# Optimization experiments

Measured on AMD Instinct MI355X. Metric: run time of the kernel, lower is better.

## Reference

```python
import jax, jax.numpy as jnp
import numpy as np

HIDDEN = 4096
NUM_HEADS = 32
HEAD_DIM = HIDDEN // NUM_HEADS  # 128, used only as softmax scale
CACHE_LEN = 100
BATCH = 8192


def setup_inputs() -> dict:
    key = jax.random.key(0)
    ks = jax.random.split(key, 7)
    return {
        "x": jax.random.normal(ks[0], (BATCH, HIDDEN), dtype=jnp.float32),
        "q_w": jax.random.normal(ks[1], (HIDDEN, HIDDEN), dtype=jnp.float32) * (1.0 / np.sqrt(HIDDEN)),
        "q_b": jax.random.normal(ks[2], (HIDDEN,), dtype=jnp.float32) * 0.01,
        "k_cache": jax.random.normal(ks[3], (CACHE_LEN, HIDDEN), dtype=jnp.float32),
        "v_cache": jax.random.normal(ks[4], (CACHE_LEN, HIDDEN), dtype=jnp.float32),
        "out_w": jax.random.normal(ks[5], (HIDDEN, HIDDEN), dtype=jnp.float32) * (1.0 / np.sqrt(HIDDEN)),
        "out_b": jax.random.normal(ks[6], (HIDDEN,), dtype=jnp.float32) * 0.01,
    }


def reference(x, q_w, q_b, k_cache, v_cache, out_w, out_b):
    # q_proj: torch Linear -> x @ W^T + b
    q = x @ q_w.T + q_b                                   # [N, H]
    # concat one zero row onto each cache (kv_len = CACHE_LEN + 1)
    k = jnp.concatenate([k_cache, jnp.zeros_like(k_cache[:1])], axis=0)  # [L+1, H]
    v = jnp.concatenate([v_cache, jnp.zeros_like(v_cache[:1])], axis=0)  # [L+1, H]
    scale = 1.0 / np.sqrt(HEAD_DIM).astype(np.float32)
    scores = (q @ k.T) * scale                            # [N, L+1]
    weights = jax.nn.softmax(scores, axis=-1)
    attn = weights @ v                                    # [N, H]
    return attn @ out_w.T + out_b                         # [N, H]
```

## Files before the change

### kernel.cpp

```cpp
#include <hip/hip_runtime.h>
#include <cstdio>

typedef __attribute__((ext_vector_type(8))) short short8;
typedef __attribute__((ext_vector_type(4))) float f32x4;


__device__ __forceinline__ unsigned short bf16r(float f) {
  union { float f; unsigned int u; } x; x.f = f;
  unsigned int r = x.u + 0x7fffu + ((x.u >> 16) & 1u);
  return (unsigned short)(r >> 16);
}

__device__ __forceinline__ float bf16f(unsigned short h) {
  union { unsigned int u; float f; } x; x.u = ((unsigned int)h) << 16;
  return x.f;
}

__device__ __forceinline__ void gload_lds16(const void* g, void* l) {
  __builtin_amdgcn_global_load_lds((const __attribute__((address_space(1))) void*)g,
                                   (__attribute__((address_space(3))) void*)l,
                                   16, 0, 0);
}

__device__ __forceinline__ short8 pack_bf16(float4 f0, float4 f1) {
  short8 h;
  h[0] = (short)bf16r(f0.x); h[1] = (short)bf16r(f0.y);
  h[2] = (short)bf16r(f0.z); h[3] = (short)bf16r(f0.w);
  h[4] = (short)bf16r(f1.x); h[5] = (short)bf16r(f1.y);
  h[6] = (short)bf16r(f1.z); h[7] = (short)bf16r(f1.w);
  return h;
}


__global__ void prep(const float* __restrict__ kc, const float* __restrict__ vc,
                     const float* __restrict__ qb,
                     unsigned short* __restrict__ kpad, unsigned short* __restrict__ vpad,
                     float* __restrict__ sbias) {
  const int b = blockIdx.x, tid = threadIdx.x;
  if (b < 4096) {
    const bool isK = b < 2048;
    const int bb = isK ? b : b - 2048;
    int idx = bb * 256 + tid;
    int row = idx >> 12;
    const float* src = isK ? kc : vc;
    float v = (row < 100) ? src[idx] : 0.f;
    (isK ? kpad : vpad)[idx] = bf16r(v);
  } else {
    const int wave = tid >> 6, lane = tid & 63;
    const int l = (b - 4096) * 4 + wave;
    float s = 0.f;
    if (l < 100) {
      for (int i = lane * 4; i < 4096; i += 256) {
        float4 k = *reinterpret_cast<const float4*>(kc + (size_t)l * 4096 + i);
        float4 q = *reinterpret_cast<const float4*>(qb + i);
        s += k.x * q.x + k.y * q.y + k.z * q.z + k.w * q.w;
      }
    }
    #pragma unroll
    for (int off = 1; off < 64; off <<= 1) s += __shfl_xor(s, off);
    if (lane == 0) sbias[l] = s;
  }
}


__device__ __forceinline__ void kq_fused_body(const unsigned short* __restrict__ Kp,
                                              const float* __restrict__ Qw,
                                              float* __restrict__ Cpart,
                                              int H, int jchunk, int js, int itile,
                                              char* smem) {
  unsigned short (*Ak)[32] = (unsigned short (*)[32])smem;
  float (*Ts)[129] = (float (*)[129])(smem + 8192);

  const int tid = threadIdx.x, wave = tid >> 6, lane = tid & 63;
  const int wm = wave >> 1, wn = wave & 1;
  const int j0 = js * jchunk;
  const int i0 = itile * 128;

  const int sr = wave * 16 + (lane >> 2);
  const int sc = (lane & 3) << 3;
  const unsigned short* Kp0 = Kp + (size_t)sr * H + j0 + sc;
  const unsigned short* Kp1 = Kp + (size_t)(64 + sr) * H + j0 + sc;
  unsigned short* AD0 = &Ak[wave * 16][0];
  unsigned short* AD1 = &Ak[64 + wave * 16][0];

  const int tj = tid >> 3;
  const int tc = (tid & 7) * 16;
  const float* Qp = Qw + (size_t)(j0 + tj) * H + i0 + tc;

  const int fr = lane & 15;
  const int kq = lane >> 4;

  f32x4 acc[4][4] = {};

  for (int jj = 0; jj < jchunk; jj += 32) {
    gload_lds16(Kp0 + jj, AD0);
    gload_lds16(Kp1 + jj, AD1);
    {
      const float* q = Qp + (size_t)jj * H;
      float4 v0 = *reinterpret_cast<const float4*>(q);
      float4 v1 = *reinterpret_cast<const float4*>(q + 4);
      float4 v2 = *reinterpret_cast<const float4*>(q + 8);
      float4 v3 = *reinterpret_cast<const float4*>(q + 12);
      Ts[tj][tc + 0]  = v0.x; Ts[tj][tc + 1]  = v0.y; Ts[tj][tc + 2]  = v0.z; Ts[tj][tc + 3]  = v0.w;
      Ts[tj][tc + 4]  = v1.x; Ts[tj][tc + 5]  = v1.y; Ts[tj][tc + 6]  = v1.z; Ts[tj][tc + 7]  = v1.w;
      Ts[tj][tc + 8]  = v2.x; Ts[tj][tc + 9]  = v2.y; Ts[tj][tc + 10] = v2.z; Ts[tj][tc + 11] = v2.w;
      Ts[tj][tc + 12] = v3.x; Ts[tj][tc + 13] = v3.y; Ts[tj][tc + 14] = v3.z; Ts[tj][tc + 15] = v3.w;
    }
    __syncthreads();

    short8 av[4];
    #pragma unroll
    for (int mi = 0; mi < 4; ++mi)
      av[mi] = *reinterpret_cast<const short8*>(&Ak[wm * 64 + mi * 16 + fr][kq * 8]);

    short8 bhi[4], blo[4];
    #pragma unroll
    for (int ni = 0; ni < 4; ++ni) {
      const int ic = wn * 64 + ni * 16 + fr;
      #pragma unroll
      for (int s = 0; s < 8; ++s) {
        float f = Ts[kq * 8 + s][ic];
        unsigned short h = bf16r(f);
        bhi[ni][s] = (short)h;
        blo[ni][s] = (short)bf16r(f - bf16f(h));
      }
    }

    #pragma unroll
    for (int mi = 0; mi < 4; ++mi)
      #pragma unroll
      for (int ni = 0; ni < 4; ++ni) {
        acc[mi][ni] = __builtin_amdgcn_mfma_f32_16x16x32_bf16(av[mi], bhi[ni], acc[mi][ni], 0, 0, 0);
        acc[mi][ni] = __builtin_amdgcn_mfma_f32_16x16x32_bf16(av[mi], blo[ni], acc[mi][ni], 0, 0, 0);
      }
    __syncthreads();
  }

  float* Cp = Cpart + (size_t)js * 128 * H;
  const int orow = (lane >> 4) * 4;
  const int ocol = lane & 15;
  #pragma unroll
  for (int mi = 0; mi < 4; ++mi) {
    #pragma unroll
    for (int ni = 0; ni < 4; ++ni) {
      size_t r0 = (size_t)wm * 64 + mi * 16 + orow;
      size_t c  = (size_t)i0 + wn * 64 + ni * 16 + ocol;
      #pragma unroll
      for (int j = 0; j < 4; ++j)
        Cp[(r0 + j) * (size_t)H + c] = acc[mi][ni][j];
    }
  }
}


template<int NB>
__device__ __forceinline__ void gemm_sv_body(const float* __restrict__ A,
                                             const unsigned short* __restrict__ B,
                                             float* __restrict__ Cpart,
                                             int M, int Kstride, int kchunk,
                                             int ks, int mblk, char* smem) {
  constexpr int FOLD = NB / 128;
  float (*As)[128][32] = (float (*)[128][32])smem;
  unsigned short (*Bs)[NB][32] = (unsigned short (*)[NB][32])(smem + 32768);

  const int tid = threadIdx.x, wave = tid >> 6, lane = tid & 63;
  const int wm = wave >> 1, wn = wave & 1;
  const size_t rowA0 = (size_t)mblk * 128;
  const int k0 = ks * kchunk;
  const int nsteps = kchunk >> 5;

  const int ar = lane >> 3;
  const int as_g = (lane & 7) ^ ar;
  const int br = lane >> 2;
  const int bs_g = (lane & 3) ^ (br & 3);

#define STAGE_SV(kt, BUF) do { \
    const int _kc = k0 + (kt) * 32; \
    _Pragma("unroll") \
    for (int j = 0; j < 4; ++j) \
      gload_lds16(A + (rowA0 + wave * 32 + j * 8 + ar) * (size_t)Kstride + _kc + as_g * 4, \
                  &As[BUF][wave * 32 + j * 8][0]); \
    _Pragma("unroll") \
    for (int j = 0; j < NB / 64; ++j) \
      gload_lds16(B + (size_t)(wave * (NB / 4) + j * 16 + br) * Kstride + _kc + bs_g * 8, \
                  &Bs[BUF][wave * (NB / 4) + j * 16][0]); \
  } while (0)

#define WAIT_STAGE do { \
    if (NB == 256) asm volatile("s_waitcnt vmcnt(8)" ::: "memory"); \
    else           asm volatile("s_waitcnt vmcnt(6)" ::: "memory"); \
  } while (0)

  const int fr = lane & 15, kq = lane >> 4;
  f32x4 acc[4][4] = {};

  STAGE_SV(0, 0);
  STAGE_SV(1, 1);
  WAIT_STAGE;
  asm volatile("" ::: "memory");
  __builtin_amdgcn_s_barrier();
  asm volatile("" ::: "memory");

  for (int k = 0; k < nsteps; ++k) {
    const int c = k & 1;

    short8 av[4], bv[4][FOLD];
    #pragma unroll
    for (int mi = 0; mi < 4; ++mi) {
      const float* rp = &As[c][wm * 64 + mi * 16 + fr][0];
      float4 f0 = *reinterpret_cast<const float4*>(rp + (((2 * kq)     ^ (fr & 7)) * 4));
      float4 f1 = *reinterpret_cast<const float4*>(rp + (((2 * kq + 1) ^ (fr & 7)) * 4));
      av[mi] = pack_bf16(f0, f1);
    }
    #pragma unroll
    for (int ni = 0; ni < 4; ++ni)
      #pragma unroll
      for (int p = 0; p < FOLD; ++p) {
        int rb = p * 128 + wn * 64 + ni * 16 + fr;
        bv[ni][p] = *reinterpret_cast<const short8*>(&Bs[c][rb][0] + ((kq ^ (fr & 3)) * 8));
      }

    asm volatile("s_waitcnt lgkmcnt(0)" ::: "memory");
    __builtin_amdgcn_s_barrier();
    asm volatile("" ::: "memory");

    const int kt2 = (k + 2 < nsteps) ? k + 2 : nsteps - 1;
    STAGE_SV(kt2, c);
    asm volatile("" ::: "memory");

    __builtin_amdgcn_s_setprio(1);
    #pragma unroll
    for (int mi = 0; mi < 4; ++mi)
      #pragma unroll
      for (int ni = 0; ni < 4; ++ni)
        #pragma unroll
        for (int p = 0; p < FOLD; ++p)
          acc[mi][ni] = __builtin_amdgcn_mfma_f32_16x16x32_bf16(av[mi], bv[ni][p], acc[mi][ni], 0, 0, 0);
    __builtin_amdgcn_s_setprio(0);

    WAIT_STAGE;
    asm volatile("" ::: "memory");
    __builtin_amdgcn_s_barrier();
    asm volatile("" ::: "memory");
  }

#undef STAGE_SV
#undef WAIT_STAGE

  float* Cp = Cpart + (size_t)ks * M * 128;
  const int orow = (lane >> 4) * 4;
  const int ocol = lane & 15;
  #pragma unroll
  for (int mi = 0; mi < 4; ++mi) {
    #pragma unroll
    for (int ni = 0; ni < 4; ++ni) {
      size_t r0 = rowA0 + wm * 64 + mi * 16 + orow;
      size_t c  = (size_t)wn * 64 + ni * 16 + ocol;
      #pragma unroll
      for (int j = 0; j < 4; ++j)
        Cp[(r0 + j) * 128 + c] = acc[mi][ni][j];
    }
  }
}


__global__ __launch_bounds__(256, 1)
void fused_kqvo(const unsigned short* __restrict__ kpad, const float* __restrict__ qw,
                float* __restrict__ KQpart,
                const float* __restrict__ outw, const unsigned short* __restrict__ vpad,
                float* __restrict__ VOpart, int H) {
  __shared__ __align__(16) char smem[49152];
  const int b = blockIdx.x;
  if (b < 256) {
    kq_fused_body(kpad, qw, KQpart, H, 512, b & 7, b >> 3, smem);
  } else {
    const int b2 = b - 256;
    gemm_sv_body<128>(outw, vpad, VOpart, H, H, 256, b2 & 15, b2 >> 4, smem);
  }
}


__global__ __launch_bounds__(256, 1)
void gemm_s(const float* __restrict__ A, const unsigned short* __restrict__ B,
            float* __restrict__ Cpart, int M, int Kstride, int kchunk) {
  __shared__ __align__(16) char smem[65536];
  gemm_sv_body<256>(A, B, Cpart, M, Kstride, kchunk, blockIdx.x, blockIdx.y, smem);
}


__global__ void reduces(const float* __restrict__ KQpart, unsigned short* __restrict__ KQ2,
                        const float* __restrict__ VOpart, unsigned short* __restrict__ VOT2) {
  const int b = blockIdx.x;
  if (b < 2048) {
    int idx = b * 256 + threadIdx.x;
    float s = 0.f;
    #pragma unroll
    for (int ks = 0; ks < 8; ++ks) s += KQpart[(size_t)ks * 128 * 4096 + idx];
    unsigned short hi = bf16r(s);
    unsigned short lo = bf16r(s - bf16f(hi));
    int l = idx >> 12, j = idx & 4095;
    KQ2[(size_t)l * 4096 + j]         = hi;
    KQ2[(size_t)(l + 128) * 4096 + j] = lo;
  } else {
    int idx = (b - 2048) * 256 + threadIdx.x;
    float s = 0.f;
    #pragma unroll
    for (int ks = 0; ks < 16; ++ks) s += VOpart[(size_t)ks * 4096 * 128 + idx];
    unsigned short hi = bf16r(s);
    unsigned short lo = bf16r(s - bf16f(hi));
    int o = idx >> 7, l = idx & 127;
    VOT2[(size_t)o * 256 + l]       = hi;
    VOT2[(size_t)o * 256 + 128 + l] = lo;
  }
}


__global__ void softmax_fused2(const float* __restrict__ Spart, const float* __restrict__ sbias,
                               unsigned short* __restrict__ W2, int rows) {
  int wave = threadIdx.x >> 6;
  int lane = threadIdx.x & 63;
  int row = blockIdx.x * (blockDim.x >> 6) + wave;
  if (row >= rows) return;
  const float scale = 0.088388347648318447f;
  float sx = 0.f, sy = 0.f;
  #pragma unroll
  for (int ks = 0; ks < 8; ++ks) {
    float2 p = reinterpret_cast<const float2*>(Spart + ((size_t)ks * rows + row) * 128)[lane];
    sx += p.x; sy += p.y;
  }
  float2 bb = reinterpret_cast<const float2*>(sbias)[lane];
  sx += bb.x; sy += bb.y;
  int c0 = lane * 2, c1 = c0 + 1;
  float s0 = (c0 <= 100) ? sx * scale : -1e30f;
  float s1 = (c1 <= 100) ? sy * scale : -1e30f;
  float m = fmaxf(s0, s1);
  #pragma unroll
  for (int off = 1; off < 64; off <<= 1) m = fmaxf(m, __shfl_xor(m, off));
  float e0 = (c0 <= 100) ? __expf(s0 - m) : 0.f;
  float e1 = (c1 <= 100) ? __expf(s1 - m) : 0.f;
  float sum = e0 + e1;
  #pragma unroll
  for (int off = 1; off < 64; off <<= 1) sum += __shfl_xor(sum, off);
  float inv = 1.f / sum;
  ushort2 o;
  o.x = bf16r(e0 * inv);
  o.y = bf16r(e1 * inv);
  reinterpret_cast<ushort2*>(W2 + (size_t)row * 256)[lane] = o;
  reinterpret_cast<ushort2*>(W2 + (size_t)row * 256 + 128)[lane] = o;
}


__global__ __launch_bounds__(256)
void gemm_final(const unsigned short* __restrict__ A,
                const unsigned short* __restrict__ B,
                const float* __restrict__ bias,
                float* __restrict__ Cout,
                int M, int N, int K) {
  __shared__ unsigned short As[128][40];
  __shared__ unsigned short Bs[128][40];

  const int tid = threadIdx.x, wave = tid >> 6, lane = tid & 63;
  const int wm = wave >> 1, wn = wave & 1;
  const size_t rowA0 = (size_t)blockIdx.y * 128;
  const size_t colB0 = (size_t)blockIdx.x * 128;

  f32x4 acc[4][4] = {};

  const int srow  = tid >> 1;
  const int shalf = (tid & 1) * 16;

  const unsigned short* Ap = A + (rowA0 + srow) * (size_t)K + shalf;
  const unsigned short* Bp = B + (colB0 + srow) * (size_t)K + shalf;

  const int fr = lane & 15;
  const int fk = (lane >> 4) << 3;

  for (int k0 = 0; k0 < K; k0 += 32) {
    short8 a0 = *reinterpret_cast<const short8*>(Ap + k0);
    short8 a1 = *reinterpret_cast<const short8*>(Ap + k0 + 8);
    short8 b0 = *reinterpret_cast<const short8*>(Bp + k0);
    short8 b1 = *reinterpret_cast<const short8*>(Bp + k0 + 8);
    *reinterpret_cast<short8*>(&As[srow][shalf])     = a0;
    *reinterpret_cast<short8*>(&As[srow][shalf + 8]) = a1;
    *reinterpret_cast<short8*>(&Bs[srow][shalf])     = b0;
    *reinterpret_cast<short8*>(&Bs[srow][shalf + 8]) = b1;
    __syncthreads();

    short8 av[4], bv[4];
    #pragma unroll
    for (int mi = 0; mi < 4; ++mi)
      av[mi] = *reinterpret_cast<const short8*>(&As[wm * 64 + mi * 16 + fr][fk]);
    #pragma unroll
    for (int ni = 0; ni < 4; ++ni)
      bv[ni] = *reinterpret_cast<const short8*>(&Bs[wn * 64 + ni * 16 + fr][fk]);
    #pragma unroll
    for (int mi = 0; mi < 4; ++mi)
      #pragma unroll
      for (int ni = 0; ni < 4; ++ni)
        acc[mi][ni] = __builtin_amdgcn_mfma_f32_16x16x32_bf16(av[mi], bv[ni], acc[mi][ni], 0, 0, 0);
    __syncthreads();
  }

  const int orow = (lane >> 4) * 4;
  const int ocol = lane & 15;
  #pragma unroll
  for (int mi = 0; mi < 4; ++mi) {
    #pragma unroll
    for (int ni = 0; ni < 4; ++ni) {
      size_t r0 = rowA0 + wm * 64 + mi * 16 + orow;
      size_t c  = colB0 + wn * 64 + ni * 16 + ocol;
      float bv_ = bias[c];
      #pragma unroll
      for (int j = 0; j < 4; ++j)
        Cout[(r0 + j) * (size_t)N + c] = acc[mi][ni][j] + bv_;
    }
  }
}


extern "C" void kernel_launch(void* const* d_in, const int* in_sizes, int n_in,
                              void* d_out, int out_size, void* d_ws, size_t ws_size,
                              hipStream_t stream) {
  const float* x       = (const float*)d_in[0];
  const float* q_w     = (const float*)d_in[1];
  const float* q_b     = (const float*)d_in[2];
  const float* k_cache = (const float*)d_in[3];
  const float* v_cache = (const float*)d_in[4];
  const float* out_w   = (const float*)d_in[5];
  const float* out_b   = (const float*)d_in[6];
  float* out = (float*)d_out;

  const int M = 8192, H = 4096;

  char* ws = (char*)d_ws;
  size_t off = 0;
  auto alloc = [&](size_t bytes) { void* p = ws + off; off += (bytes + 255) & ~(size_t)255; return p; };
  unsigned short* kpad   = (unsigned short*)alloc((size_t)128 * H * 2);
  unsigned short* vpad   = (unsigned short*)alloc((size_t)128 * H * 2);
  float*          sbias  = (float*)alloc(128 * 4);
  unsigned short* KQ2    = (unsigned short*)alloc((size_t)256 * H * 2);
  unsigned short* W2     = (unsigned short*)alloc((size_t)M * 256 * 2);
  unsigned short* VOT2   = (unsigned short*)alloc((size_t)H * 256 * 2);
  float*          KQpart = (float*)alloc((size_t)8 * 128 * H * 4);
  float*          VOpart = (float*)alloc((size_t)16 * H * 128 * 4);
  float*          Spart  = VOpart;
  if (ws_size < off) { fprintf(stderr, "ws too small: need %zu have %zu\n", off, ws_size); return; }

  prep<<<4128, 256, 0, stream>>>(k_cache, v_cache, q_b, kpad, vpad, sbias);

  fused_kqvo<<<768, 256, 0, stream>>>(kpad, q_w, KQpart, out_w, vpad, VOpart, H);

  reduces<<<4096, 256, 0, stream>>>(KQpart, KQ2, VOpart, VOT2);

  gemm_s<<<dim3(8, 64), 256, 0, stream>>>(x, KQ2, Spart, M, H, 512);

  softmax_fused2<<<M / 4, 256, 0, stream>>>(Spart, sbias, W2, M);

  gemm_final<<<dim3(32, 64), 256, 0, stream>>>(W2, VOT2, out_b, out, M, H, 256);
}
```

Before: 162.0 us.

## Reschedule kernels so V·outW GEMM runs alongside the x·KQ GEMM

Result: slower. 178.7 us (+10.3%).

```diff
diff --git a/kernel.cpp b/kernel.cpp
--- a/kernel.cpp
+++ b/kernel.cpp
@@ -265,42 +265,79 @@
 
 
 __global__ __launch_bounds__(256, 1)
-void fused_kqvo(const unsigned short* __restrict__ kpad, const float* __restrict__ qw,
-                float* __restrict__ KQpart,
-                const float* __restrict__ outw, const unsigned short* __restrict__ vpad,
-                float* __restrict__ VOpart, int H) {
-  __shared__ __align__(16) char smem[49152];
+void kq_only(const unsigned short* __restrict__ kpad, const float* __restrict__ qw,
+             float* __restrict__ KQpart, int H) {
+  __shared__ __align__(16) char smem[25088];
+  kq_fused_body(kpad, qw, KQpart, H, 512, blockIdx.x & 7, blockIdx.x >> 3, smem);
+}
+
+
+__global__ void kq_reduce(const float* __restrict__ KQpart, unsigned short* __restrict__ KQ2) {
+  int idx = blockIdx.x * blockDim.x + threadIdx.x;
+  if (idx >= 128 * 4096) return;
+  float s = 0.f;
+  #pragma unroll
+  for (int ks = 0; ks < 8; ++ks) s += KQpart[(size_t)ks * 128 * 4096 + idx];
+  unsigned short hi = bf16r(s);
+  unsigned short lo = bf16r(s - bf16f(hi));
+  int l = idx >> 12, j = idx & 4095;
+  KQ2[(size_t)l * 4096 + j]         = hi;
+  KQ2[(size_t)(l + 128) * 4096 + j] = lo;
+}
+
+
+__global__ __launch_bounds__(256, 1)
+void sv_combo(const float* __restrict__ x, const unsigned short* __restrict__ KQ2,
+              float* __restrict__ Spart,
+              const float* __restrict__ outw, const unsigned short* __restrict__ vpad,
+              float* __restrict__ VOpart, int M, int H) {
+  __shared__ __align__(16) char smem[65536];
   const int b = blockIdx.x;
-  if (b < 256) {
-    kq_fused_body(kpad, qw, KQpart, H, 512, b & 7, b >> 3, smem);
+  if (b < 512) {
+    gemm_sv_body<256>(x, KQ2, Spart, M, H, 512, b & 7, b >> 3, smem);
   } else {
-    const int b2 = b - 256;
+    const int b2 = b - 512;
     gemm_sv_body<128>(outw, vpad, VOpart, H, H, 256, b2 & 15, b2 >> 4, smem);
   }
 }
 
 
-__global__ __launch_bounds__(256, 1)
-void gemm_s(const float* __restrict__ A, const unsigned short* __restrict__ B,
-            float* __restrict__ Cpart, int M, int Kstride, int kchunk) {
-  __shared__ __align__(16) char smem[65536];
-  gemm_sv_body<256>(A, B, Cpart, M, Kstride, kchunk, blockIdx.x, blockIdx.y, smem);
-}
-
-
-__global__ void reduces(const float* __restrict__ KQpart, unsigned short* __restrict__ KQ2,
-                        const float* __restrict__ VOpart, unsigned short* __restrict__ VOT2) {
+__global__ void soft_vored(const float* __restrict__ Spart, const float* __restrict__ sbias,
+                           unsigned short* __restrict__ W2,
+                           const float* __restrict__ VOpart, unsigned short* __restrict__ VOT2,
+                           int rows) {
   const int b = blockIdx.x;
   if (b < 2048) {
-    int idx = b * 256 + threadIdx.x;
-    float s = 0.f;
-    #pragma unroll
-    for (int ks = 0; ks < 8; ++ks) s += KQpart[(size_t)ks * 128 * 4096 + idx];
-    unsigned short hi = bf16r(s);
-    unsigned short lo = bf16r(s - bf16f(hi));
-    int l = idx >> 12, j = idx & 4095;
-    KQ2[(size_t)l * 4096 + j]         = hi;
-    KQ2[(size_t)(l + 128) * 4096 + j] = lo;
+    int wave = threadIdx.x >> 6;
+    int lane = threadIdx.x & 63;
+    int row = b * 4 + wave;
+    if (row >= rows) return;
+    const float scale = 0.088388347648318447f;
+    float sx = 0.f, sy = 0.f;
+    #pragma unroll
+    for (int ks = 0; ks < 8; ++ks) {
+      float2 p = reinterpret_cast<const float2*>(Spart + ((size_t)ks * rows + row) * 128)[lane];
+      sx += p.x; sy += p.y;
+    }
+    float2 bb = reinterpret_cast<const float2*>(sbias)[lane];
+    sx += bb.x; sy += bb.y;
+    int c0 = lane * 2, c1 = c0 + 1;
+    float s0 = (c0 <= 100) ? sx * scale : -1e30f;
+    float s1 = (c1 <= 100) ? sy * scale : -1e30f;
+    float m = fmaxf(s0, s1);
+    #pragma unroll
+    for (int off = 1; off < 64; off <<= 1) m = fmaxf(m, __shfl_xor(m, off));
+    float e0 = (c0 <= 100) ? __expf(s0 - m) : 0.f;
+    float e1 = (c1 <= 100) ? __expf(s1 - m) : 0.f;
+    float sum = e0 + e1;
+    #pragma unroll
+    for (int off = 1; off < 64; off <<= 1) sum += __shfl_xor(sum, off);
+    float inv = 1.f / sum;
+    ushort2 o;
+    o.x = bf16r(e0 * inv);
+    o.y = bf16r(e1 * inv);
+    reinterpret_cast<ushort2*>(W2 + (size_t)row * 256)[lane] = o;
+    reinterpret_cast<ushort2*>(W2 + (size_t)row * 256 + 128)[lane] = o;
   } else {
     int idx = (b - 2048) * 256 + threadIdx.x;
     float s = 0.f;
@@ -312,41 +349,6 @@
     VOT2[(size_t)o * 256 + l]       = hi;
     VOT2[(size_t)o * 256 + 128 + l] = lo;
   }
-}
-
-
-__global__ void softmax_fused2(const float* __restrict__ Spart, const float* __restrict__ sbias,
-                               unsigned short* __restrict__ W2, int rows) {
-  int wave = threadIdx.x >> 6;
-  int lane = threadIdx.x & 63;
-  int row = blockIdx.x * (blockDim.x >> 6) + wave;
-  if (row >= rows) return;
-  const float scale = 0.088388347648318447f;
-  float sx = 0.f, sy = 0.f;
-  #pragma unroll
-  for (int ks = 0; ks < 8; ++ks) {
-    float2 p = reinterpret_cast<const float2*>(Spart + ((size_t)ks * rows + row) * 128)[lane];
-    sx += p.x; sy += p.y;
-  }
-  float2 bb = reinterpret_cast<const float2*>(sbias)[lane];
-  sx += bb.x; sy += bb.y;
-  int c0 = lane * 2, c1 = c0 + 1;
-  float s0 = (c0 <= 100) ? sx * scale : -1e30f;
-  float s1 = (c1 <= 100) ? sy * scale : -1e30f;
-  float m = fmaxf(s0, s1);
-  #pragma unroll
-  for (int off = 1; off < 64; off <<= 1) m = fmaxf(m, __shfl_xor(m, off));
-  float e0 = (c0 <= 100) ? __expf(s0 - m) : 0.f;
-  float e1 = (c1 <= 100) ? __expf(s1 - m) : 0.f;
-  float sum = e0 + e1;
-  #pragma unroll
-  for (int off = 1; off < 64; off <<= 1) sum += __shfl_xor(sum, off);
-  float inv = 1.f / sum;
-  ushort2 o;
-  o.x = bf16r(e0 * inv);
-  o.y = bf16r(e1 * inv);
-  reinterpret_cast<ushort2*>(W2 + (size_t)row * 256)[lane] = o;
-  reinterpret_cast<ushort2*>(W2 + (size_t)row * 256 + 128)[lane] = o;
 }
 
 
@@ -443,18 +445,18 @@
   unsigned short* VOT2   = (unsigned short*)alloc((size_t)H * 256 * 2);
   float*          KQpart = (float*)alloc((size_t)8 * 128 * H * 4);
   float*          VOpart = (float*)alloc((size_t)16 * H * 128 * 4);
-  float*          Spart  = VOpart;
+  float*          Spart  = (float*)alloc((size_t)8 * M * 128 * 4);
   if (ws_size < off) { fprintf(stderr, "ws too small: need %zu have %zu\n", off, ws_size); return; }
 
   prep<<<4128, 256, 0, stream>>>(k_cache, v_cache, q_b, kpad, vpad, sbias);
 
-  fused_kqvo<<<768, 256, 0, stream>>>(kpad, q_w, KQpart, out_w, vpad, VOpart, H);
-
-  reduces<<<4096, 256, 0, stream>>>(KQpart, KQ2, VOpart, VOT2);
-
-  gemm_s<<<dim3(8, 64), 256, 0, stream>>>(x, KQ2, Spart, M, H, 512);
-
-  softmax_fused2<<<M / 4, 256, 0, stream>>>(Spart, sbias, W2, M);
+  kq_only<<<256, 256, 0, stream>>>(kpad, q_w, KQpart, H);
+
+  kq_reduce<<<2048, 256, 0, stream>>>(KQpart, KQ2);
+
+  sv_combo<<<1024, 256, 0, stream>>>(x, KQ2, Spart, out_w, vpad, VOpart, M, H);
+
+  soft_vored<<<4096, 256, 0, stream>>>(Spart, sbias, W2, VOpart, VOT2, M);
 
   gemm_final<<<dim3(32, 64), 256, 0, stream>>>(W2, VOT2, out_b, out, M, H, 256);
 }
```
